# Performance work log

Hardware: AMD Instinct MI355X
Metric: run time of the kernel (lower is better)

## Reference

```python
import jax, jax.numpy as jnp
import numpy as np

N = 8192
NFEAT = 256
NHID = 64


def setup_inputs() -> dict:
    key = jax.random.key(0)
    k1, k2, k3, k4, k5 = jax.random.split(key, 5)
    x = jax.random.normal(k1, (N, NFEAT), dtype=jnp.float32)
    # symmetric-normalized-ish dense adjacency (random sparse-like weights)
    adj = jax.random.uniform(k2, (N, N), dtype=jnp.float32)
    W1 = jax.random.normal(k3, (NFEAT, NHID), dtype=jnp.float32) * (1.0 / np.sqrt(NFEAT))
    W2 = jax.random.normal(k4, (NHID, NHID), dtype=jnp.float32) * (1.0 / np.sqrt(NHID))
    W3 = jax.random.normal(k5, (NHID, NHID), dtype=jnp.float32) * (1.0 / np.sqrt(NHID))
    return {"x": x, "adj": adj, "W1": W1, "W2": W2, "W3": W3}


def _gcn(x, adj, W):
    # eval mode: dropout is identity. support = x @ W ; out = adj @ support
    return adj @ (x @ W)


def reference(x, adj, W1, W2, W3):
    h1 = jax.nn.relu(_gcn(x, adj, W1))         # [N, nhid]
    mu = _gcn(h1, adj, W2)                      # [N, nhid]
    logvar = _gcn(h1, adj, W3)                  # [N, nhid]
    z = mu                                      # eval: reparameterize returns mu
    recon = z @ z.T                             # [N, N] inner-product decode, act=identity
    return recon, mu, logvar
```

## Files before the change

kernel.cpp:

```cpp
#include <hip/hip_runtime.h>

typedef __bf16 bf16;
typedef __attribute__((ext_vector_type(4))) __bf16 bf16x4;
typedef __attribute__((ext_vector_type(8))) __bf16 bf16x8;
typedef __attribute__((ext_vector_type(4))) float f32x4;

#define MFMA16(a, b, c) __builtin_amdgcn_mfma_f32_16x16x32_bf16((a), (b), (c), 0, 0, 0)

constexpr int BM  = 128;
constexpr int BK  = 64;
constexpr int LDT = 72;

constexpr int N    = 8192;
constexpr int FEAT = 256;
constexpr int HID  = 64;
constexpr int KSPLIT = 16;

template <int NCOL, bool AF32, bool WRITEB>
__global__ __launch_bounds__(256) void gcn_mm(const float* __restrict__ A,
                                              const bf16* __restrict__ Abf, int K,
                                              const bf16* __restrict__ Bt,
                                              float* __restrict__ Cpart, int ktiles,
                                              bf16* __restrict__ Aout) {
  __shared__ bf16 As[BM * LDT];
  __shared__ bf16 Bs[NCOL * LDT];
  const int tid = threadIdx.x;
  const int lane = tid & 63;
  const int wave = tid >> 6;
  const int i0 = blockIdx.x * BM;
  const int kbase = blockIdx.y * ktiles * BK;

  f32x4 acc[2][NCOL / 16] = {};

  for (int kt = 0; kt < ktiles; ++kt) {
    const int k0 = kbase + kt * BK;
    if constexpr (AF32) {
      const int rr = tid >> 4, c4 = tid & 15;
#pragma unroll
      for (int s = 0; s < 8; ++s) {
        const int row = rr + s * 16;
        const float4 v = *reinterpret_cast<const float4*>(&A[(size_t)(i0 + row) * K + k0 + c4 * 4]);
        bf16x4 o;
        o[0] = (bf16)v.x; o[1] = (bf16)v.y; o[2] = (bf16)v.z; o[3] = (bf16)v.w;
        *reinterpret_cast<bf16x4*>(&As[row * LDT + c4 * 4]) = o;
        if constexpr (WRITEB)
          *reinterpret_cast<bf16x4*>(&Aout[(size_t)(i0 + row) * K + k0 + c4 * 4]) = o;
      }
    } else {
#pragma unroll
      for (int s = 0; s < 4; ++s) {
        const int idx = tid + s * 256;
        const int row = idx >> 3, q = idx & 7;
        *reinterpret_cast<bf16x8*>(&As[row * LDT + q * 8]) =
            *reinterpret_cast<const bf16x8*>(&Abf[(size_t)(i0 + row) * K + k0 + q * 8]);
      }
    }
    {
#pragma unroll
      for (int s = 0; s < NCOL / 32; ++s) {
        const int idx = tid + s * 256;
        const int n = idx >> 3, q = idx & 7;
        *reinterpret_cast<bf16x8*>(&Bs[n * LDT + q * 8]) =
            *reinterpret_cast<const bf16x8*>(&Bt[(size_t)n * K + k0 + q * 8]);
      }
    }
    __syncthreads();
    const int rA = wave * 32 + (lane & 15);
#pragma unroll
    for (int kk = 0; kk < 2; ++kk) {
      const int kb = kk * 32 + ((lane >> 4) << 3);
      const bf16x8 a0 = *reinterpret_cast<const bf16x8*>(&As[rA * LDT + kb]);
      const bf16x8 a1 = *reinterpret_cast<const bf16x8*>(&As[(rA + 16) * LDT + kb]);
#pragma unroll
      for (int n = 0; n < NCOL / 16; ++n) {
        const bf16x8 b = *reinterpret_cast<const bf16x8*>(&Bs[(n * 16 + (lane & 15)) * LDT + kb]);
        acc[0][n] = MFMA16(a0, b, acc[0][n]);
        acc[1][n] = MFMA16(a1, b, acc[1][n]);
      }
    }
    __syncthreads();
  }
  float* Cp = Cpart + (size_t)blockIdx.y * N * NCOL;
  const int r4 = (lane >> 4) << 2, col = lane & 15;
#pragma unroll
  for (int m = 0; m < 2; ++m)
#pragma unroll
    for (int n = 0; n < NCOL / 16; ++n)
#pragma unroll
      for (int r = 0; r < 4; ++r)
        Cp[(size_t)(i0 + wave * 32 + m * 16 + r4 + r) * NCOL + n * 16 + col] = acc[m][n][r];
}

__global__ void prep_w1t(const float* __restrict__ W1, bf16* __restrict__ W1T) {
  const int idx = blockIdx.x * 256 + threadIdx.x;
  const int j = idx >> 8, k = idx & 255;
  W1T[idx] = (bf16)W1[k * HID + j];
}

__global__ __launch_bounds__(256) void transpose_bf16_64(const float* __restrict__ in,
                                                         bf16* __restrict__ out) {
  __shared__ float t[64][65];
  const int i0 = blockIdx.x * 64;
  const int tid = threadIdx.x;
#pragma unroll
  for (int s = 0; s < 4; ++s) {
    const int idx = tid + s * 256;
    const int row = idx >> 4, c4 = idx & 15;
    const float4 v = *reinterpret_cast<const float4*>(&in[(size_t)(i0 + row) * HID + c4 * 4]);
    t[row][c4 * 4 + 0] = v.x; t[row][c4 * 4 + 1] = v.y;
    t[row][c4 * 4 + 2] = v.z; t[row][c4 * 4 + 3] = v.w;
  }
  __syncthreads();
#pragma unroll
  for (int s = 0; s < 2; ++s) {
    const int idx = tid + s * 256;
    const int j = idx >> 3, q = idx & 7;
    bf16x8 o;
#pragma unroll
    for (int e = 0; e < 8; ++e) o[e] = (bf16)t[q * 8 + e][j];
    *reinterpret_cast<bf16x8*>(&out[(size_t)j * N + i0 + q * 8]) = o;
  }
}

__global__ __launch_bounds__(256) void reduce_relu_w23(const float* __restrict__ pB,
                                                       const float* __restrict__ W2,
                                                       const float* __restrict__ W3,
                                                       bf16* __restrict__ s23T) {
  __shared__ float Hs[64][65];
  __shared__ float Ws[64][128];
  const int i0 = blockIdx.x * 64;
  const int tid = threadIdx.x;
#pragma unroll
  for (int s = 0; s < 32; ++s) {
    const int idx = tid + s * 256;
    const int c = idx >> 7, j = idx & 127;
    Ws[c][j] = (j < 64) ? W2[c * HID + j] : W3[c * HID + (j - 64)];
  }
#pragma unroll
  for (int s8 = 0; s8 < 16; ++s8) {
    const int idx = tid + s8 * 256;
    const int r = idx >> 6, c = idx & 63;
    const size_t off = (size_t)(i0 + r) * HID + c;
    float a = 0.0f;
#pragma unroll
    for (int s = 0; s < KSPLIT; ++s) a += pB[(size_t)s * N * HID + off];
    Hs[r][c] = fmaxf(a, 0.0f);
  }
  __syncthreads();
  const int j = tid & 127, ih = tid >> 7;
  for (int ii = ih; ii < 64; ii += 2) {
    float a = 0.0f;
#pragma unroll
    for (int c = 0; c < 64; ++c) a += Hs[ii][c] * Ws[c][j];
    s23T[(size_t)j * N + i0 + ii] = (bf16)a;
  }
}

__global__ __launch_bounds__(256) void reduce_mu_lv(const float* __restrict__ pC,
                                                    float* __restrict__ mu,
                                                    float* __restrict__ lv) {
  const int idx = blockIdx.x * 256 + threadIdx.x;
  const int g4 = idx * 4;
  const int i = g4 >> 7, j = g4 & 127;
  float4 a = {0.f, 0.f, 0.f, 0.f};
#pragma unroll
  for (int s = 0; s < KSPLIT; ++s) {
    const float4 v = *reinterpret_cast<const float4*>(&pC[(size_t)s * N * 2 * HID + g4]);
    a.x += v.x; a.y += v.y; a.z += v.z; a.w += v.w;
  }
  float* dst = (j < 64) ? &mu[i * HID + j] : &lv[i * HID + (j - 64)];
  *reinterpret_cast<float4*>(dst) = a;
}

__global__ __launch_bounds__(256) void recon_mm(const float* __restrict__ mu,
                                                float* __restrict__ out) {
  __shared__ bf16 Am[BM * LDT];
  __shared__ bf16 Bm[BM * LDT];
  const int tid = threadIdx.x, lane = tid & 63, wave = tid >> 6;
  const int i0 = blockIdx.x * 128, j0 = blockIdx.y * 128;
  {
    const int rr = tid >> 4, c4 = tid & 15;
#pragma unroll
    for (int s = 0; s < 8; ++s) {
      const int row = rr + s * 16;
      const float4 v = *reinterpret_cast<const float4*>(&mu[(size_t)(i0 + row) * HID + c4 * 4]);
      bf16x4 o;
      o[0] = (bf16)v.x; o[1] = (bf16)v.y; o[2] = (bf16)v.z; o[3] = (bf16)v.w;
      *reinterpret_cast<bf16x4*>(&Am[row * LDT + c4 * 4]) = o;
      const float4 w = *reinterpret_cast<const float4*>(&mu[(size_t)(j0 + row) * HID + c4 * 4]);
      bf16x4 p;
      p[0] = (bf16)w.x; p[1] = (bf16)w.y; p[2] = (bf16)w.z; p[3] = (bf16)w.w;
      *reinterpret_cast<bf16x4*>(&Bm[row * LDT + c4 * 4]) = p;
    }
  }
  __syncthreads();
  f32x4 acc[2][8] = {};
  const int rA = wave * 32 + (lane & 15);
#pragma unroll
  for (int kk = 0; kk < 2; ++kk) {
    const int kb = kk * 32 + ((lane >> 4) << 3);
    const bf16x8 a0 = *reinterpret_cast<const bf16x8*>(&Am[rA * LDT + kb]);
    const bf16x8 a1 = *reinterpret_cast<const bf16x8*>(&Am[(rA + 16) * LDT + kb]);
#pragma unroll
    for (int n = 0; n < 8; ++n) {
      const bf16x8 b = *reinterpret_cast<const bf16x8*>(&Bm[(n * 16 + (lane & 15)) * LDT + kb]);
      acc[0][n] = MFMA16(a0, b, acc[0][n]);
      acc[1][n] = MFMA16(a1, b, acc[1][n]);
    }
  }
  const int r4 = (lane >> 4) << 2, c = lane & 15;
#pragma unroll
  for (int m = 0; m < 2; ++m)
#pragma unroll
    for (int n = 0; n < 8; ++n)
#pragma unroll
      for (int r = 0; r < 4; ++r)
        out[(size_t)(i0 + wave * 32 + m * 16 + r4 + r) * N + j0 + n * 16 + c] = acc[m][n][r];
}

extern "C" void kernel_launch(void* const* d_in, const int* in_sizes, int n_in, void* d_out,
                              int out_size, void* d_ws, size_t ws_size, hipStream_t stream) {
  const float* x   = (const float*)d_in[0];
  const float* adj = (const float*)d_in[1];
  const float* W1  = (const float*)d_in[2];
  const float* W2  = (const float*)d_in[3];
  const float* W3  = (const float*)d_in[4];

  float* out    = (float*)d_out;
  float* recon  = out;
  float* mu_out = out + (size_t)N * N;
  float* lv_out = mu_out + (size_t)N * HID;

  char* scr    = (char*)d_out;
  bf16*  S1T   = (bf16*)(scr + 0);
  float* s1acc = (float*)(scr + (1u << 20));
  bf16*  s23T  = (bf16*)(scr + (3u << 20));
  bf16*  W1T   = (bf16*)(scr + (5u << 20));
  float* pB    = (float*)(scr + (6u << 20));
  float* pC    = (float*)(scr + (38u << 20));
  bf16*  adjB  = (bf16*)(scr + (102u << 20));

  prep_w1t<<<64, 256, 0, stream>>>(W1, W1T);
  gcn_mm<64, true, false><<<dim3(64, 1), 256, 0, stream>>>(x, nullptr, FEAT, W1T, s1acc,
                                                           FEAT / BK, nullptr);
  transpose_bf16_64<<<128, 256, 0, stream>>>(s1acc, S1T);
  gcn_mm<64, true, true><<<dim3(64, KSPLIT), 256, 0, stream>>>(adj, nullptr, N, S1T, pB,
                                                               (N / KSPLIT) / BK, adjB);
  reduce_relu_w23<<<128, 256, 0, stream>>>(pB, W2, W3, s23T);
  gcn_mm<128, false, false><<<dim3(64, KSPLIT), 256, 0, stream>>>(nullptr, adjB, N, s23T, pC,
                                                                  (N / KSPLIT) / BK, nullptr);
  reduce_mu_lv<<<1024, 256, 0, stream>>>(pC, mu_out, lv_out);
  recon_mm<<<dim3(64, 64), 256, 0, stream>>>(mu_out, recon);
}
```

Before: 276.6 us.

## Convert adjacency to bf16 in a separate streaming pass and halve split-K

Moves the fp32-to-bf16 conversion of the adjacency out of the first aggregation GEMM into a dedicated grid-stride streaming kernel. Both adjacency GEMMs then read the bf16 copy. The split-K factor drops from 16 to 8, which halves the partial-sum buffers and the reduction traffic but gives fewer blocks. The cost is an extra read of the bf16 adjacency in the first GEMM plus one more launch, traded for simpler GEMM loads and less partial traffic.

```diff
diff --git a/kernel.cpp b/kernel.cpp
--- a/kernel.cpp
+++ b/kernel.cpp
@@ -14,14 +14,27 @@
 constexpr int N    = 8192;
 constexpr int FEAT = 256;
 constexpr int HID  = 64;
-constexpr int KSPLIT = 16;
-
-template <int NCOL, bool AF32, bool WRITEB>
+constexpr int KSPLIT = 8;
+
+__global__ __launch_bounds__(256) void convert_adj(const float* __restrict__ in,
+                                                   bf16* __restrict__ out) {
+  const size_t stride = (size_t)gridDim.x * 256;
+  const size_t nchunk = (size_t)N * N / 8;
+  for (size_t c = (size_t)blockIdx.x * 256 + threadIdx.x; c < nchunk; c += stride) {
+    const float4 v0 = *reinterpret_cast<const float4*>(&in[c * 8]);
+    const float4 v1 = *reinterpret_cast<const float4*>(&in[c * 8 + 4]);
+    bf16x8 o;
+    o[0] = (bf16)v0.x; o[1] = (bf16)v0.y; o[2] = (bf16)v0.z; o[3] = (bf16)v0.w;
+    o[4] = (bf16)v1.x; o[5] = (bf16)v1.y; o[6] = (bf16)v1.z; o[7] = (bf16)v1.w;
+    *reinterpret_cast<bf16x8*>(&out[c * 8]) = o;
+  }
+}
+
+template <int NCOL, bool AF32>
 __global__ __launch_bounds__(256) void gcn_mm(const float* __restrict__ A,
                                               const bf16* __restrict__ Abf, int K,
                                               const bf16* __restrict__ Bt,
-                                              float* __restrict__ Cpart, int ktiles,
-                                              bf16* __restrict__ Aout) {
+                                              float* __restrict__ Cpart, int ktiles) {
   __shared__ bf16 As[BM * LDT];
   __shared__ bf16 Bs[NCOL * LDT];
   const int tid = threadIdx.x;
@@ -43,8 +56,6 @@
         bf16x4 o;
         o[0] = (bf16)v.x; o[1] = (bf16)v.y; o[2] = (bf16)v.z; o[3] = (bf16)v.w;
         *reinterpret_cast<bf16x4*>(&As[row * LDT + c4 * 4]) = o;
-        if constexpr (WRITEB)
-          *reinterpret_cast<bf16x4*>(&Aout[(size_t)(i0 + row) * K + k0 + c4 * 4]) = o;
       }
     } else {
 #pragma unroll
@@ -237,18 +248,19 @@
   bf16*  s23T  = (bf16*)(scr + (3u << 20));
   bf16*  W1T   = (bf16*)(scr + (5u << 20));
   float* pB    = (float*)(scr + (6u << 20));
-  float* pC    = (float*)(scr + (38u << 20));
+  float* pC    = (float*)(scr + (22u << 20));
   bf16*  adjB  = (bf16*)(scr + (102u << 20));
 
+  convert_adj<<<2048, 256, 0, stream>>>(adj, adjB);
+
   prep_w1t<<<64, 256, 0, stream>>>(W1, W1T);
-  gcn_mm<64, true, false><<<dim3(64, 1), 256, 0, stream>>>(x, nullptr, FEAT, W1T, s1acc,
-                                                           FEAT / BK, nullptr);
+  gcn_mm<64, true><<<dim3(64, 1), 256, 0, stream>>>(x, nullptr, FEAT, W1T, s1acc, FEAT / BK);
   transpose_bf16_64<<<128, 256, 0, stream>>>(s1acc, S1T);
-  gcn_mm<64, true, true><<<dim3(64, KSPLIT), 256, 0, stream>>>(adj, nullptr, N, S1T, pB,
-                                                               (N / KSPLIT) / BK, adjB);
+  gcn_mm<64, false><<<dim3(64, KSPLIT), 256, 0, stream>>>(nullptr, adjB, N, S1T, pB,
+                                                          (N / KSPLIT) / BK);
   reduce_relu_w23<<<128, 256, 0, stream>>>(pB, W2, W3, s23T);
-  gcn_mm<128, false, false><<<dim3(64, KSPLIT), 256, 0, stream>>>(nullptr, adjB, N, s23T, pC,
-                                                                  (N / KSPLIT) / BK, nullptr);
+  gcn_mm<128, false><<<dim3(64, KSPLIT), 256, 0, stream>>>(nullptr, adjB, N, s23T, pC,
+                                                           (N / KSPLIT) / BK);
   reduce_mu_lv<<<1024, 256, 0, stream>>>(pC, mu_out, lv_out);
   recon_mm<<<dim3(64, 64), 256, 0, stream>>>(mu_out, recon);
 }
```

After: 268.2 us. 1.03x faster.

## Reassociate second GCN layer to compute adj@h1 once, then apply W2/W3

Applied to the files above, without the earlier changes.

The second and third GCN layers are reassociated as (adj @ h1) @ [W2|W3], so the big adjacency product uses 64 output columns instead of 128. The bf16 copy of adj is dropped and the second pass rereads fp32 adj and converts it again. KSPLIT also goes from 16 to 8, and the small W2/W3 product is fused into the partial-sum reduction. This cuts MFMA work and the 128MB bf16 write/read, but the second pass now reads 256MB of fp32 adj instead of 128MB of bf16, and the change of association may shift rounding.

```diff
diff --git a/kernel.cpp b/kernel.cpp
--- a/kernel.cpp
+++ b/kernel.cpp
@@ -14,27 +14,24 @@
 constexpr int N    = 8192;
 constexpr int FEAT = 256;
 constexpr int HID  = 64;
-constexpr int KSPLIT = 16;
-
-template <int NCOL, bool AF32, bool WRITEB>
-__global__ __launch_bounds__(256) void gcn_mm(const float* __restrict__ A,
-                                              const bf16* __restrict__ Abf, int K,
+constexpr int KSPLIT = 8;
+
+__global__ __launch_bounds__(256) void gcn_mm(const float* __restrict__ A, int K,
                                               const bf16* __restrict__ Bt,
-                                              float* __restrict__ Cpart, int ktiles,
-                                              bf16* __restrict__ Aout) {
+                                              float* __restrict__ Cpart, int ktiles) {
   __shared__ bf16 As[BM * LDT];
-  __shared__ bf16 Bs[NCOL * LDT];
+  __shared__ bf16 Bs[64 * LDT];
   const int tid = threadIdx.x;
   const int lane = tid & 63;
   const int wave = tid >> 6;
   const int i0 = blockIdx.x * BM;
   const int kbase = blockIdx.y * ktiles * BK;
 
-  f32x4 acc[2][NCOL / 16] = {};
+  f32x4 acc[2][4] = {};
 
   for (int kt = 0; kt < ktiles; ++kt) {
     const int k0 = kbase + kt * BK;
-    if constexpr (AF32) {
+    {
       const int rr = tid >> 4, c4 = tid & 15;
 #pragma unroll
       for (int s = 0; s < 8; ++s) {
@@ -43,26 +40,15 @@
         bf16x4 o;
         o[0] = (bf16)v.x; o[1] = (bf16)v.y; o[2] = (bf16)v.z; o[3] = (bf16)v.w;
         *reinterpret_cast<bf16x4*>(&As[row * LDT + c4 * 4]) = o;
-        if constexpr (WRITEB)
-          *reinterpret_cast<bf16x4*>(&Aout[(size_t)(i0 + row) * K + k0 + c4 * 4]) = o;
       }
-    } else {
-#pragma unroll
-      for (int s = 0; s < 4; ++s) {
-        const int idx = tid + s * 256;
-        const int row = idx >> 3, q = idx & 7;
-        *reinterpret_cast<bf16x8*>(&As[row * LDT + q * 8]) =
-            *reinterpret_cast<const bf16x8*>(&Abf[(size_t)(i0 + row) * K + k0 + q * 8]);
-      }
     }
     {
-#pragma unroll
-      for (int s = 0; s < NCOL / 32; ++s) {
-        const int idx = tid + s * 256;
-        const int n = idx >> 3, q = idx & 7;
-        *reinterpret_cast<bf16x8*>(&Bs[n * LDT + q * 8]) =
-            *reinterpret_cast<const bf16x8*>(&Bt[(size_t)n * K + k0 + q * 8]);
-      }
+      const int idx = tid * 2;
+      const int n = idx >> 3, q = idx & 7;
+      *reinterpret_cast<bf16x8*>(&Bs[n * LDT + q * 8]) =
+          *reinterpret_cast<const bf16x8*>(&Bt[(size_t)n * K + k0 + q * 8]);
+      *reinterpret_cast<bf16x8*>(&Bs[n * LDT + (q + 1) * 8]) =
+          *reinterpret_cast<const bf16x8*>(&Bt[(size_t)n * K + k0 + (q + 1) * 8]);
     }
     __syncthreads();
     const int rA = wave * 32 + (lane & 15);
@@ -72,7 +58,7 @@
       const bf16x8 a0 = *reinterpret_cast<const bf16x8*>(&As[rA * LDT + kb]);
       const bf16x8 a1 = *reinterpret_cast<const bf16x8*>(&As[(rA + 16) * LDT + kb]);
 #pragma unroll
-      for (int n = 0; n < NCOL / 16; ++n) {
+      for (int n = 0; n < 4; ++n) {
         const bf16x8 b = *reinterpret_cast<const bf16x8*>(&Bs[(n * 16 + (lane & 15)) * LDT + kb]);
         acc[0][n] = MFMA16(a0, b, acc[0][n]);
         acc[1][n] = MFMA16(a1, b, acc[1][n]);
@@ -80,15 +66,15 @@
     }
     __syncthreads();
   }
-  float* Cp = Cpart + (size_t)blockIdx.y * N * NCOL;
+  float* Cp = Cpart + (size_t)blockIdx.y * N * HID;
   const int r4 = (lane >> 4) << 2, col = lane & 15;
 #pragma unroll
   for (int m = 0; m < 2; ++m)
 #pragma unroll
-    for (int n = 0; n < NCOL / 16; ++n)
+    for (int n = 0; n < 4; ++n)
 #pragma unroll
       for (int r = 0; r < 4; ++r)
-        Cp[(size_t)(i0 + wave * 32 + m * 16 + r4 + r) * NCOL + n * 16 + col] = acc[m][n][r];
+        Cp[(size_t)(i0 + wave * 32 + m * 16 + r4 + r) * HID + n * 16 + col] = acc[m][n][r];
 }
 
 __global__ void prep_w1t(const float* __restrict__ W1, bf16* __restrict__ W1T) {
@@ -122,10 +108,42 @@
   }
 }
 
-__global__ __launch_bounds__(256) void reduce_relu_w23(const float* __restrict__ pB,
+__global__ __launch_bounds__(256) void reduce_relu_T(const float* __restrict__ pB,
+                                                     bf16* __restrict__ h1T) {
+  __shared__ float t[64][65];
+  const int i0 = blockIdx.x * 64;
+  const int tid = threadIdx.x;
+#pragma unroll
+  for (int s = 0; s < 4; ++s) {
+    const int idx = tid + s * 256;
+    const int row = idx >> 4, c4 = idx & 15;
+    const size_t off = (size_t)(i0 + row) * HID + c4 * 4;
+    float4 a = {0.f, 0.f, 0.f, 0.f};
+#pragma unroll
+    for (int sp = 0; sp < KSPLIT; ++sp) {
+      const float4 v = *reinterpret_cast<const float4*>(&pB[(size_t)sp * N * HID + off]);
+      a.x += v.x; a.y += v.y; a.z += v.z; a.w += v.w;
+    }
+    t[row][c4 * 4 + 0] = fmaxf(a.x, 0.f); t[row][c4 * 4 + 1] = fmaxf(a.y, 0.f);
+    t[row][c4 * 4 + 2] = fmaxf(a.z, 0.f); t[row][c4 * 4 + 3] = fmaxf(a.w, 0.f);
+  }
+  __syncthreads();
+#pragma unroll
+  for (int s = 0; s < 2; ++s) {
+    const int idx = tid + s * 256;
+    const int j = idx >> 3, q = idx & 7;
+    bf16x8 o;
+#pragma unroll
+    for (int e = 0; e < 8; ++e) o[e] = (bf16)t[q * 8 + e][j];
+    *reinterpret_cast<bf16x8*>(&h1T[(size_t)j * N + i0 + q * 8]) = o;
+  }
+}
+
+__global__ __launch_bounds__(256) void reduce_w23_mulv(const float* __restrict__ pC,
                                                        const float* __restrict__ W2,
                                                        const float* __restrict__ W3,
-                                                       bf16* __restrict__ s23T) {
+                                                       float* __restrict__ mu,
+                                                       float* __restrict__ lv) {
   __shared__ float Hs[64][65];
   __shared__ float Ws[64][128];
   const int i0 = blockIdx.x * 64;
@@ -143,8 +161,8 @@
     const size_t off = (size_t)(i0 + r) * HID + c;
     float a = 0.0f;
 #pragma unroll
-    for (int s = 0; s < KSPLIT; ++s) a += pB[(size_t)s * N * HID + off];
-    Hs[r][c] = fmaxf(a, 0.0f);
+    for (int sp = 0; sp < KSPLIT; ++sp) a += pC[(size_t)sp * N * HID + off];
+    Hs[r][c] = a;
   }
   __syncthreads();
   const int j = tid & 127, ih = tid >> 7;
@@ -152,24 +170,11 @@
     float a = 0.0f;
 #pragma unroll
     for (int c = 0; c < 64; ++c) a += Hs[ii][c] * Ws[c][j];
-    s23T[(size_t)j * N + i0 + ii] = (bf16)a;
-  }
-}
-
-__global__ __launch_bounds__(256) void reduce_mu_lv(const float* __restrict__ pC,
-                                                    float* __restrict__ mu,
-                                                    float* __restrict__ lv) {
-  const int idx = blockIdx.x * 256 + threadIdx.x;
-  const int g4 = idx * 4;
-  const int i = g4 >> 7, j = g4 & 127;
-  float4 a = {0.f, 0.f, 0.f, 0.f};
-#pragma unroll
-  for (int s = 0; s < KSPLIT; ++s) {
-    const float4 v = *reinterpret_cast<const float4*>(&pC[(size_t)s * N * 2 * HID + g4]);
-    a.x += v.x; a.y += v.y; a.z += v.z; a.w += v.w;
-  }
-  float* dst = (j < 64) ? &mu[i * HID + j] : &lv[i * HID + (j - 64)];
-  *reinterpret_cast<float4*>(dst) = a;
+    if (j < 64)
+      mu[(size_t)(i0 + ii) * HID + j] = a;
+    else
+      lv[(size_t)(i0 + ii) * HID + (j - 64)] = a;
+  }
 }
 
 __global__ __launch_bounds__(256) void recon_mm(const float* __restrict__ mu,
@@ -234,21 +239,17 @@
   char* scr    = (char*)d_out;
   bf16*  S1T   = (bf16*)(scr + 0);
   float* s1acc = (float*)(scr + (1u << 20));
-  bf16*  s23T  = (bf16*)(scr + (3u << 20));
-  bf16*  W1T   = (bf16*)(scr + (5u << 20));
-  float* pB    = (float*)(scr + (6u << 20));
-  float* pC    = (float*)(scr + (38u << 20));
-  bf16*  adjB  = (bf16*)(scr + (102u << 20));
+  bf16*  h1T   = (bf16*)(scr + (3u << 20));
+  bf16*  W1T   = (bf16*)(scr + (4u << 20));
+  float* pB    = (float*)(scr + (5u << 20));
+  float* pC    = (float*)(scr + (21u << 20));
 
   prep_w1t<<<64, 256, 0, stream>>>(W1, W1T);
-  gcn_mm<64, true, false><<<dim3(64, 1), 256, 0, stream>>>(x, nullptr, FEAT, W1T, s1acc,
-                                                           FEAT / BK, nullptr);
+  gcn_mm<<<dim3(64, 1), 256, 0, stream>>>(x, FEAT, W1T, s1acc, FEAT / BK);
   transpose_bf16_64<<<128, 256, 0, stream>>>(s1acc, S1T);
-  gcn_mm<64, true, true><<<dim3(64, KSPLIT), 256, 0, stream>>>(adj, nullptr, N, S1T, pB,
-                                                               (N / KSPLIT) / BK, adjB);
-  reduce_relu_w23<<<128, 256, 0, stream>>>(pB, W2, W3, s23T);
-  gcn_mm<128, false, false><<<dim3(64, KSPLIT), 256, 0, stream>>>(nullptr, adjB, N, s23T, pC,
-                                                                  (N / KSPLIT) / BK, nullptr);
-  reduce_mu_lv<<<1024, 256, 0, stream>>>(pC, mu_out, lv_out);
+  gcn_mm<<<dim3(64, KSPLIT), 256, 0, stream>>>(adj, N, S1T, pB, (N / KSPLIT) / BK);
+  reduce_relu_T<<<128, 256, 0, stream>>>(pB, h1T);
+  gcn_mm<<<dim3(64, KSPLIT), 256, 0, stream>>>(adj, N, h1T, pC, (N / KSPLIT) / BK);
+  reduce_w23_mulv<<<128, 256, 0, stream>>>(pC, W2, W3, mu_out, lv_out);
   recon_mm<<<dim3(64, 64), 256, 0, stream>>>(mu_out, recon);
 }
```

After: 323.8 us. +17.1%, slower.
